# Optimization experiments

Measured on AMD Instinct MI355X. Metric: run time of the kernel, lower is better.

## Reference

```python
import jax, jax.numpy as jnp
import numpy as np

N_NODES = 100000
N_EDGES = 3200000
IN_CH = 32
HID = 16


def setup_inputs() -> dict:
    key = jax.random.key(0)
    ks = jax.random.split(key, 8)
    x = jax.random.normal(ks[0], (N_NODES, IN_CH), dtype=jnp.float32)
    edge_index = jax.random.randint(ks[1], (2, N_EDGES), 0, N_NODES, dtype=jnp.int64)
    s1 = 1.0 / np.sqrt(IN_CH)
    s2 = 1.0 / np.sqrt(HID)
    Wl1 = jax.random.normal(ks[2], (HID, IN_CH), dtype=jnp.float32) * s1
    Wr1 = jax.random.normal(ks[3], (HID, IN_CH), dtype=jnp.float32) * s1
    b1 = jnp.zeros((HID,), dtype=jnp.float32)
    Wl2 = jax.random.normal(ks[4], (1, HID), dtype=jnp.float32) * s2
    Wr2 = jax.random.normal(ks[5], (1, HID), dtype=jnp.float32) * s2
    b2 = jnp.zeros((1,), dtype=jnp.float32)
    return {"x": x, "edge_index": edge_index, "Wl1": Wl1, "Wr1": Wr1,
            "b1": b1, "Wl2": Wl2, "Wr2": Wr2, "b2": b2}


def _sage_conv(h, src, dst, deg_inv, Wl, Wr, b):
    # mean aggregation of source features at destination nodes
    msg_sum = jax.ops.segment_sum(h[src], dst, num_segments=N_NODES)  # [N, F]
    agg = msg_sum * deg_inv[:, None]
    # lin_l(agg) + lin_r(h): lin_l carries the bias (PyG SAGEConv convention)
    return agg @ Wl.T + b + h @ Wr.T


def reference(x, edge_index, Wl1, Wr1, b1, Wl2, Wr2, b2):
    src = edge_index[0]
    dst = edge_index[1]
    deg = jax.ops.segment_sum(jnp.ones((N_EDGES,), dtype=x.dtype), dst,
                              num_segments=N_NODES)
    deg_inv = 1.0 / jnp.maximum(deg, 1.0)  # mean; nodes w/o in-edges get 0 agg

    h = _sage_conv(x, src, dst, deg_inv, Wl1, Wr1, b1)
    h = jax.nn.relu(h)
    # F.dropout in eval mode -> identity
    out = _sage_conv(h, src, dst, deg_inv, Wl2, Wr2, b2)
    return out.squeeze(-1)  # [N]
```

## Files before the change

### kernel.cpp

```cpp
#include <hip/hip_runtime.h>

#define N_NODES 100000
#define N_EDGES 3200000
#define NB 1024
#define BKN 98
#define RSZ 3968
#define TILE 6250
#define NTILES 512
#define MAXIT 13
#define MAXB 8


__device__ __forceinline__ float bf2f_lo(unsigned int w) {
  return __uint_as_float(w << 16);
}
__device__ __forceinline__ float bf2f_hi(unsigned int w) {
  return __uint_as_float(w & 0xFFFF0000u);
}
__device__ __forceinline__ unsigned short f2bf(float f) {
  unsigned int b = __float_as_uint(f);
  return (unsigned short)((b + 0x7FFFu + ((b >> 16) & 1u)) >> 16);
}

__global__ __launch_bounds__(256) void k_proj1(
    const float* __restrict__ x, const float* __restrict__ Wl1,
    const float* __restrict__ Wr1, const float* __restrict__ b1,
    unsigned short* __restrict__ p1h, float* __restrict__ q1b,
    int* __restrict__ gcur) {
  __shared__ float sWl[512];
  __shared__ float sWr[512];
  __shared__ float sb[16];
  const int t = threadIdx.x;
  if (t < 64) {
    const int gi = blockIdx.x * 64 + t;
    if (gi < NB * 16) gcur[gi] = 0;
  }
  for (int i = t; i < 512; i += 256) {
    sWl[i] = Wl1[i];
    sWr[i] = Wr1[i];
  }
  if (t < 16) sb[t] = b1[t];
  __syncthreads();

  const int n = blockIdx.x * 256 + t;
  if (n >= N_NODES) return;

  float xr[32];
  const float4* xp = (const float4*)(x + (size_t)n * 32);
#pragma unroll
  for (int j = 0; j < 8; ++j) {
    float4 v = xp[j];
    xr[4 * j + 0] = v.x;
    xr[4 * j + 1] = v.y;
    xr[4 * j + 2] = v.z;
    xr[4 * j + 3] = v.w;
  }
  float pv[16], qv[16];
#pragma unroll
  for (int hh = 0; hh < 16; ++hh) {
    float a = 0.f, b = 0.f;
#pragma unroll
    for (int i = 0; i < 32; ++i) {
      a = fmaf(xr[i], sWl[hh * 32 + i], a);
      b = fmaf(xr[i], sWr[hh * 32 + i], b);
    }
    pv[hh] = a;
    qv[hh] = b + sb[hh];
  }
  unsigned int w[8];
#pragma unroll
  for (int j = 0; j < 8; ++j)
    w[j] = (unsigned int)f2bf(pv[2 * j]) |
           ((unsigned int)f2bf(pv[2 * j + 1]) << 16);
  uint4* pp = (uint4*)(p1h + (size_t)n * 16);
  pp[0] = make_uint4(w[0], w[1], w[2], w[3]);
  pp[1] = make_uint4(w[4], w[5], w[6], w[7]);
  float4* qp = (float4*)(q1b + (size_t)n * 16);
#pragma unroll
  for (int j = 0; j < 4; ++j)
    qp[j] = make_float4(qv[4 * j], qv[4 * j + 1], qv[4 * j + 2], qv[4 * j + 3]);
}

__global__ __launch_bounds__(512) void k_bscatter(const int* __restrict__ ei,
                                                  int* __restrict__ gcur,
                                                  int* __restrict__ recs) {
  __shared__ int hist[1024];
  __shared__ int delta[NB];
  __shared__ int seg[512];
  __shared__ int stage[TILE];
  __shared__ unsigned short bid[TILE + 6];
  const int t = threadIdx.x;
  for (int i = t; i < 1024; i += 512) hist[i] = 0;
  __syncthreads();

  const int tb = blockIdx.x * TILE;
  int rec[MAXIT], aux[MAXIT];
#pragma unroll
  for (int i = 0; i < MAXIT; ++i) {
    const int pos = t + i * 512;
    if (pos < TILE) {
      const int e = tb + pos;
      const int s = ei[e];
      const int d = ei[N_EDGES + e];
      const int k = (int)((unsigned)d / (unsigned)BKN);
      const int rank = atomicAdd(&hist[k], 1);
      rec[i] = ((d - k * BKN) << 17) | s;
      aux[i] = (k << 16) | rank;
    } else {
      aux[i] = -1;
    }
  }
  __syncthreads();

  const int s0 = hist[2 * t], s1 = hist[2 * t + 1];
  const int my = s0 + s1;
  seg[t] = my;
  __syncthreads();
#pragma unroll
  for (int o = 1; o < 512; o <<= 1) {
    const int a = (t >= o) ? seg[t - o] : 0;
    __syncthreads();
    seg[t] += a;
    __syncthreads();
  }
  const int ex = seg[t] - my;
  hist[2 * t] = ex;
  hist[2 * t + 1] = ex + s0;
  {
    const int b = 2 * t;
    if (s0) delta[b] = b * RSZ + atomicAdd(&gcur[b * 16], s0) - ex;
    if (s1)
      delta[b + 1] =
          (b + 1) * RSZ + atomicAdd(&gcur[(b + 1) * 16], s1) - (ex + s0);
  }
  __syncthreads();

#pragma unroll
  for (int i = 0; i < MAXIT; ++i) {
    if (aux[i] >= 0) stage[hist[aux[i] >> 16] + (aux[i] & 0xFFFF)] = rec[i];
  }
  for (int k2 = t; k2 < NB; k2 += 512) {
    const int st = hist[k2];
    const int en = (k2 == NB - 1) ? TILE : hist[k2 + 1];
    for (int p = st; p < en; ++p) bid[p] = (unsigned short)k2;
  }
  __syncthreads();

  for (int pos = t; pos < TILE; pos += 512) {
    const int bb = bid[pos];
    const int idx = delta[bb] + pos;
    if (idx < (bb + 1) * RSZ) recs[idx] = stage[pos];
  }
}

__global__ __launch_bounds__(512, 8) void k_sortagg1(
    const int* __restrict__ gcur, const int* __restrict__ recs,
    const unsigned short* __restrict__ p1h, const float* __restrict__ q1b,
    const float* __restrict__ Wl2, const float* __restrict__ Wr2,
    float* __restrict__ p2, float* __restrict__ r2,
    float* __restrict__ deg_inv) {
  __shared__ int hist[128];
  __shared__ int nstart[128];
  __shared__ int ssort[RSZ];
  __shared__ float sWl[16], sWr[16];
  const int t = threadIdx.x;
  const int kb = blockIdx.x;
  const int b0 = kb * RSZ;
  const int gend = b0 + min(gcur[kb * 16], RSZ);
  if (t < 128) hist[t] = 0;
  if (t < 16) {
    sWl[t] = Wl2[t];
    sWr[t] = Wr2[t];
  }
  __syncthreads();

  int rc[MAXB], ax[MAXB];
#pragma unroll
  for (int i = 0; i < MAXB; ++i) {
    const int r = b0 + t + i * 512;
    if (r < gend) {
      const int rv = recs[r];
      const int local = rv >> 17;
      const int rank = atomicAdd(&hist[local], 1);
      rc[i] = rv & 0x1FFFF;
      ax[i] = (local << 13) | rank;
    } else {
      ax[i] = -1;
    }
  }
  __syncthreads();

  {
    const int v = (t < 128) ? hist[t] : 0;
    if (t < 128) nstart[t] = v;
    __syncthreads();
#pragma unroll
    for (int o = 1; o < 128; o <<= 1) {
      const int a = (t < 128 && t >= o) ? nstart[t - o] : 0;
      __syncthreads();
      if (t < 128) nstart[t] += a;
      __syncthreads();
    }
    if (t < 128) nstart[t] -= v;
  }
  __syncthreads();

#pragma unroll
  for (int i = 0; i < MAXB; ++i) {
    if (ax[i] >= 0) ssort[nstart[ax[i] >> 13] + (ax[i] & 0x1FFF)] = rc[i];
  }
  __syncthreads();

  const int quad = t & 3;
  const int half = quad & 1;
  const int epar = quad >> 1;
  const unsigned short* pb = p1h + half * 8;
  const int local = t >> 2;
  if (local < BKN) {
    const int n = kb * BKN + local;
    if (n < N_NODES) {
      const int st = nstart[local];
      const int k = hist[local];

      float acc[8];
#pragma unroll
      for (int i = 0; i < 8; ++i) acc[i] = 0.f;
      int j = epar;
      for (; j + 6 < k; j += 8) {
        const int s0 = ssort[st + j], s1 = ssort[st + j + 2],
                  s2 = ssort[st + j + 4], s3 = ssort[st + j + 6];
        const uint4 w0 = *(const uint4*)(pb + (size_t)s0 * 16);
        const uint4 w1 = *(const uint4*)(pb + (size_t)s1 * 16);
        const uint4 w2 = *(const uint4*)(pb + (size_t)s2 * 16);
        const uint4 w3 = *(const uint4*)(pb + (size_t)s3 * 16);
        acc[0] +=
            (bf2f_lo(w0.x) + bf2f_lo(w1.x)) + (bf2f_lo(w2.x) + bf2f_lo(w3.x));
        acc[1] +=
            (bf2f_hi(w0.x) + bf2f_hi(w1.x)) + (bf2f_hi(w2.x) + bf2f_hi(w3.x));
        acc[2] +=
            (bf2f_lo(w0.y) + bf2f_lo(w1.y)) + (bf2f_lo(w2.y) + bf2f_lo(w3.y));
        acc[3] +=
            (bf2f_hi(w0.y) + bf2f_hi(w1.y)) + (bf2f_hi(w2.y) + bf2f_hi(w3.y));
        acc[4] +=
            (bf2f_lo(w0.z) + bf2f_lo(w1.z)) + (bf2f_lo(w2.z) + bf2f_lo(w3.z));
        acc[5] +=
            (bf2f_hi(w0.z) + bf2f_hi(w1.z)) + (bf2f_hi(w2.z) + bf2f_hi(w3.z));
        acc[6] +=
            (bf2f_lo(w0.w) + bf2f_lo(w1.w)) + (bf2f_lo(w2.w) + bf2f_lo(w3.w));
        acc[7] +=
            (bf2f_hi(w0.w) + bf2f_hi(w1.w)) + (bf2f_hi(w2.w) + bf2f_hi(w3.w));
      }
      for (; j < k; j += 2) {
        const uint4 w = *(const uint4*)(pb + (size_t)ssort[st + j] * 16);
        acc[0] += bf2f_lo(w.x);
        acc[1] += bf2f_hi(w.x);
        acc[2] += bf2f_lo(w.y);
        acc[3] += bf2f_hi(w.y);
        acc[4] += bf2f_lo(w.z);
        acc[5] += bf2f_hi(w.z);
        acc[6] += bf2f_lo(w.w);
        acc[7] += bf2f_hi(w.w);
      }
#pragma unroll
      for (int i = 0; i < 8; ++i) acc[i] += __shfl_xor(acc[i], 2);

      const float di = 1.f / fmaxf((float)k, 1.f);
      const float4* qp = (const float4*)(q1b + (size_t)n * 16 + half * 8);
      const float4 qa = qp[0], qb = qp[1];
      float h[8];
      h[0] = fmaxf(fmaf(acc[0], di, qa.x), 0.f);
      h[1] = fmaxf(fmaf(acc[1], di, qa.y), 0.f);
      h[2] = fmaxf(fmaf(acc[2], di, qa.z), 0.f);
      h[3] = fmaxf(fmaf(acc[3], di, qa.w), 0.f);
      h[4] = fmaxf(fmaf(acc[4], di, qb.x), 0.f);
      h[5] = fmaxf(fmaf(acc[5], di, qb.y), 0.f);
      h[6] = fmaxf(fmaf(acc[6], di, qb.z), 0.f);
      h[7] = fmaxf(fmaf(acc[7], di, qb.w), 0.f);
      float pa = 0.f, pbv = 0.f;
#pragma unroll
      for (int i = 0; i < 8; ++i) {
        pa = fmaf(h[i], sWl[half * 8 + i], pa);
        pbv = fmaf(h[i], sWr[half * 8 + i], pbv);
      }
      pa += __shfl_xor(pa, 1);
      pbv += __shfl_xor(pbv, 1);
      if (quad == 0) {
        p2[n] = pa;
        r2[n] = pbv;
        deg_inv[n] = di;
      }
    }
  }
}

__global__ __launch_bounds__(512, 8) void k_agg2out(
    const int* __restrict__ gcur, const int* __restrict__ recs,
    const float* __restrict__ p2, const float* __restrict__ r2,
    const float* __restrict__ deg_inv, const float* __restrict__ b2,
    float* __restrict__ out) {
  __shared__ float acc[BKN];
  const int t = threadIdx.x;
  const int kb = blockIdx.x;
  if (t < BKN) acc[t] = 0.f;
  __syncthreads();

  const int b0 = kb * RSZ;
  const int cnt = min(gcur[kb * 16], RSZ);
  int r = t;
  for (; r + 1536 < cnt; r += 2048) {
    const int rv0 = recs[b0 + r];
    const int rv1 = recs[b0 + r + 512];
    const int rv2 = recs[b0 + r + 1024];
    const int rv3 = recs[b0 + r + 1536];
    const float v0 = p2[rv0 & 0x1FFFF];
    const float v1 = p2[rv1 & 0x1FFFF];
    const float v2 = p2[rv2 & 0x1FFFF];
    const float v3 = p2[rv3 & 0x1FFFF];
    atomicAdd(&acc[rv0 >> 17], v0);
    atomicAdd(&acc[rv1 >> 17], v1);
    atomicAdd(&acc[rv2 >> 17], v2);
    atomicAdd(&acc[rv3 >> 17], v3);
  }
  for (; r < cnt; r += 512) {
    const int rv = recs[b0 + r];
    atomicAdd(&acc[rv >> 17], p2[rv & 0x1FFFF]);
  }
  __syncthreads();

  if (t < BKN) {
    const int n = kb * BKN + t;
    if (n < N_NODES) out[n] = fmaf(acc[t], deg_inv[n], r2[n] + b2[0]);
  }
}

extern "C" void kernel_launch(void* const* d_in, const int* in_sizes, int n_in,
                              void* d_out, int out_size, void* d_ws,
                              size_t ws_size, hipStream_t stream) {
  const float* x   = (const float*)d_in[0];
  const int*   ei  = (const int*)d_in[1];
  const float* Wl1 = (const float*)d_in[2];
  const float* Wr1 = (const float*)d_in[3];
  const float* b1  = (const float*)d_in[4];
  const float* Wl2 = (const float*)d_in[5];
  const float* Wr2 = (const float*)d_in[6];
  const float* b2  = (const float*)d_in[7];
  float* out = (float*)d_out;

  const size_t N = N_NODES;
  int* wi = (int*)d_ws;
  int* gcur = wi;
  int* recs = wi + NB * 16;
  unsigned short* p1h = (unsigned short*)(recs + (size_t)NB * RSZ);
  float* q1b     = (float*)(p1h + 16 * N);
  float* p2      = q1b + 16 * N;
  float* r2      = p2 + N;
  float* deg_inv = r2 + N;

  k_proj1<<<(N_NODES + 255) / 256, 256, 0, stream>>>(x, Wl1, Wr1, b1, p1h,
                                                     q1b, gcur);
  k_bscatter<<<NTILES, 512, 0, stream>>>(ei, gcur, recs);
  k_sortagg1<<<NB, 512, 0, stream>>>(gcur, recs, p1h, q1b, Wl2, Wr2, p2, r2,
                                     deg_inv);
  k_agg2out<<<NB, 512, 0, stream>>>(gcur, recs, p2, r2, deg_inv, b2, out);
}
```

Before: 172.0 us.

## Fuse projection with edge scatter and merge layer aggregations via grid barrier

Layer-1 projection and the bucket scatter now run as one launch: one group of blocks scatters edges while another group projects nodes. The two aggregation stages are merged into a cooperative kernel that uses a global atomic barrier, so the sorted source lists, r2 and deg_inv stay in shared memory and are not written out and read back. The gcur reset moves to a memset, and the 128-entry prefix scan now uses wave shuffles. This removes two launches and some global traffic, but adds a spin-wait grid barrier and the memset, and falls back to the old path if the cooperative launch fails.

Measured after the change: 356.7 us. 107% more time.

```diff
diff --git a/kernel.cpp b/kernel.cpp
--- a/kernel.cpp
+++ b/kernel.cpp
@@ -9,6 +9,7 @@
 #define NTILES 512
 #define MAXIT 13
 #define MAXB 8
+#define PROJ_BLOCKS 196
 
 
 __device__ __forceinline__ float bf2f_lo(unsigned int w) {
@@ -17,32 +18,101 @@
 __device__ __forceinline__ float bf2f_hi(unsigned int w) {
   return __uint_as_float(w & 0xFFFF0000u);
 }
-__device__ __forceinline__ unsigned short f2bf(float f) {
+__device__ __forceinline__ unsigned int f2bf(float f) {
   unsigned int b = __float_as_uint(f);
-  return (unsigned short)((b + 0x7FFFu + ((b >> 16) & 1u)) >> 16);
-}
-
-__global__ __launch_bounds__(256) void k_proj1(
-    const float* __restrict__ x, const float* __restrict__ Wl1,
-    const float* __restrict__ Wr1, const float* __restrict__ b1,
-    unsigned short* __restrict__ p1h, float* __restrict__ q1b,
-    int* __restrict__ gcur) {
-  __shared__ float sWl[512];
-  __shared__ float sWr[512];
-  __shared__ float sb[16];
+  return (b + 0x7FFFu + ((b >> 16) & 1u)) >> 16;
+}
+
+__global__ __launch_bounds__(512, 8) void k_scatterproj(
+    const float* __restrict__ x, const int* __restrict__ ei,
+    const float* __restrict__ Wl1, const float* __restrict__ Wr1,
+    const float* __restrict__ b1, unsigned short* __restrict__ p1h,
+    float* __restrict__ q1b, int* __restrict__ gcur, int* __restrict__ recs) {
+  __shared__ union {
+    struct {
+      int hist[1024];
+      int delta[NB];
+      int seg[512];
+      int stage[TILE];
+      unsigned short bid[TILE + 6];
+    } s;
+    struct { float Wl[512], Wr[512], b[16]; } w;
+  } u;
   const int t = threadIdx.x;
-  if (t < 64) {
-    const int gi = blockIdx.x * 64 + t;
-    if (gi < NB * 16) gcur[gi] = 0;
-  }
-  for (int i = t; i < 512; i += 256) {
-    sWl[i] = Wl1[i];
-    sWr[i] = Wr1[i];
-  }
-  if (t < 16) sb[t] = b1[t];
-  __syncthreads();
-
-  const int n = blockIdx.x * 256 + t;
+  const int kb = blockIdx.x;
+
+  if (kb < NTILES) {
+    for (int i = t; i < 1024; i += 512) u.s.hist[i] = 0;
+    __syncthreads();
+
+    const int tb = kb * TILE;
+    int rec[MAXIT], aux[MAXIT];
+#pragma unroll
+    for (int i = 0; i < MAXIT; ++i) {
+      const int pos = t + i * 512;
+      if (pos < TILE) {
+        const int e = tb + pos;
+        const int s = ei[e];
+        const int d = ei[N_EDGES + e];
+        const int k = (int)((unsigned)d / (unsigned)BKN);
+        const int rank = atomicAdd(&u.s.hist[k], 1);
+        rec[i] = ((d - k * BKN) << 17) | s;
+        aux[i] = (k << 16) | rank;
+      } else {
+        aux[i] = -1;
+      }
+    }
+    __syncthreads();
+
+    const int s0 = u.s.hist[2 * t], s1 = u.s.hist[2 * t + 1];
+    const int my = s0 + s1;
+    u.s.seg[t] = my;
+    __syncthreads();
+#pragma unroll
+    for (int o = 1; o < 512; o <<= 1) {
+      const int a = (t >= o) ? u.s.seg[t - o] : 0;
+      __syncthreads();
+      u.s.seg[t] += a;
+      __syncthreads();
+    }
+    const int ex = u.s.seg[t] - my;
+    u.s.hist[2 * t] = ex;
+    u.s.hist[2 * t + 1] = ex + s0;
+    {
+      const int b = 2 * t;
+      if (s0) u.s.delta[b] = b * RSZ + atomicAdd(&gcur[b * 16], s0) - ex;
+      if (s1)
+        u.s.delta[b + 1] =
+            (b + 1) * RSZ + atomicAdd(&gcur[(b + 1) * 16], s1) - (ex + s0);
+    }
+    __syncthreads();
+
+#pragma unroll
+    for (int i = 0; i < MAXIT; ++i) {
+      if (aux[i] >= 0)
+        u.s.stage[u.s.hist[aux[i] >> 16] + (aux[i] & 0xFFFF)] = rec[i];
+    }
+    for (int k2 = t; k2 < NB; k2 += 512) {
+      const int st = u.s.hist[k2];
+      const int en = (k2 == NB - 1) ? TILE : u.s.hist[k2 + 1];
+      for (int p = st; p < en; ++p) u.s.bid[p] = (unsigned short)k2;
+    }
+    __syncthreads();
+
+    for (int pos = t; pos < TILE; pos += 512) {
+      const int bb = u.s.bid[pos];
+      const int idx = u.s.delta[bb] + pos;
+      if (idx < (bb + 1) * RSZ) recs[idx] = u.s.stage[pos];
+    }
+    return;
+  }
+
+  u.w.Wl[t] = Wl1[t];
+  u.w.Wr[t] = Wr1[t];
+  if (t < 16) u.w.b[t] = b1[t];
+  __syncthreads();
+
+  const int n = (kb - NTILES) * 512 + t;
   if (n >= N_NODES) return;
 
   float xr[32];
@@ -55,116 +125,40 @@
     xr[4 * j + 2] = v.z;
     xr[4 * j + 3] = v.w;
   }
-  float pv[16], qv[16];
-#pragma unroll
-  for (int hh = 0; hh < 16; ++hh) {
-    float a = 0.f, b = 0.f;
-#pragma unroll
-    for (int i = 0; i < 32; ++i) {
-      a = fmaf(xr[i], sWl[hh * 32 + i], a);
-      b = fmaf(xr[i], sWr[hh * 32 + i], b);
-    }
-    pv[hh] = a;
-    qv[hh] = b + sb[hh];
-  }
-  unsigned int w[8];
-#pragma unroll
-  for (int j = 0; j < 8; ++j)
-    w[j] = (unsigned int)f2bf(pv[2 * j]) |
-           ((unsigned int)f2bf(pv[2 * j + 1]) << 16);
-  uint4* pp = (uint4*)(p1h + (size_t)n * 16);
-  pp[0] = make_uint4(w[0], w[1], w[2], w[3]);
-  pp[1] = make_uint4(w[4], w[5], w[6], w[7]);
-  float4* qp = (float4*)(q1b + (size_t)n * 16);
-#pragma unroll
-  for (int j = 0; j < 4; ++j)
-    qp[j] = make_float4(qv[4 * j], qv[4 * j + 1], qv[4 * j + 2], qv[4 * j + 3]);
-}
-
-__global__ __launch_bounds__(512) void k_bscatter(const int* __restrict__ ei,
-                                                  int* __restrict__ gcur,
-                                                  int* __restrict__ recs) {
-  __shared__ int hist[1024];
-  __shared__ int delta[NB];
-  __shared__ int seg[512];
-  __shared__ int stage[TILE];
-  __shared__ unsigned short bid[TILE + 6];
-  const int t = threadIdx.x;
-  for (int i = t; i < 1024; i += 512) hist[i] = 0;
-  __syncthreads();
-
-  const int tb = blockIdx.x * TILE;
-  int rec[MAXIT], aux[MAXIT];
-#pragma unroll
-  for (int i = 0; i < MAXIT; ++i) {
-    const int pos = t + i * 512;
-    if (pos < TILE) {
-      const int e = tb + pos;
-      const int s = ei[e];
-      const int d = ei[N_EDGES + e];
-      const int k = (int)((unsigned)d / (unsigned)BKN);
-      const int rank = atomicAdd(&hist[k], 1);
-      rec[i] = ((d - k * BKN) << 17) | s;
-      aux[i] = (k << 16) | rank;
-    } else {
-      aux[i] = -1;
-    }
-  }
-  __syncthreads();
-
-  const int s0 = hist[2 * t], s1 = hist[2 * t + 1];
-  const int my = s0 + s1;
-  seg[t] = my;
-  __syncthreads();
-#pragma unroll
-  for (int o = 1; o < 512; o <<= 1) {
-    const int a = (t >= o) ? seg[t - o] : 0;
-    __syncthreads();
-    seg[t] += a;
-    __syncthreads();
-  }
-  const int ex = seg[t] - my;
-  hist[2 * t] = ex;
-  hist[2 * t + 1] = ex + s0;
-  {
-    const int b = 2 * t;
-    if (s0) delta[b] = b * RSZ + atomicAdd(&gcur[b * 16], s0) - ex;
-    if (s1)
-      delta[b + 1] =
-          (b + 1) * RSZ + atomicAdd(&gcur[(b + 1) * 16], s1) - (ex + s0);
-  }
-  __syncthreads();
-
-#pragma unroll
-  for (int i = 0; i < MAXIT; ++i) {
-    if (aux[i] >= 0) stage[hist[aux[i] >> 16] + (aux[i] & 0xFFFF)] = rec[i];
-  }
-  for (int k2 = t; k2 < NB; k2 += 512) {
-    const int st = hist[k2];
-    const int en = (k2 == NB - 1) ? TILE : hist[k2 + 1];
-    for (int p = st; p < en; ++p) bid[p] = (unsigned short)k2;
-  }
-  __syncthreads();
-
-  for (int pos = t; pos < TILE; pos += 512) {
-    const int bb = bid[pos];
-    const int idx = delta[bb] + pos;
-    if (idx < (bb + 1) * RSZ) recs[idx] = stage[pos];
-  }
-}
-
-__global__ __launch_bounds__(512, 8) void k_sortagg1(
-    const int* __restrict__ gcur, const int* __restrict__ recs,
-    const unsigned short* __restrict__ p1h, const float* __restrict__ q1b,
-    const float* __restrict__ Wl2, const float* __restrict__ Wr2,
-    float* __restrict__ p2, float* __restrict__ r2,
-    float* __restrict__ deg_inv) {
-  __shared__ int hist[128];
-  __shared__ int nstart[128];
-  __shared__ int ssort[RSZ];
-  __shared__ float sWl[16], sWr[16];
-  const int t = threadIdx.x;
-  const int kb = blockIdx.x;
+#pragma unroll
+  for (int ch = 0; ch < 2; ++ch) {
+    float pv[8], qv[8];
+#pragma unroll
+    for (int h2 = 0; h2 < 8; ++h2) {
+      const int hh = ch * 8 + h2;
+      float a = 0.f, b = 0.f;
+#pragma unroll
+      for (int i = 0; i < 32; ++i) {
+        a = fmaf(xr[i], u.w.Wl[hh * 32 + i], a);
+        b = fmaf(xr[i], u.w.Wr[hh * 32 + i], b);
+      }
+      pv[h2] = a;
+      qv[h2] = b + u.w.b[hh];
+    }
+    unsigned int w[4];
+#pragma unroll
+    for (int j = 0; j < 4; ++j)
+      w[j] = f2bf(pv[2 * j]) | (f2bf(pv[2 * j + 1]) << 16);
+    ((uint4*)(p1h + (size_t)n * 16))[ch] = make_uint4(w[0], w[1], w[2], w[3]);
+    float4* qp = (float4*)(q1b + (size_t)n * 16) + 2 * ch;
+    qp[0] = make_float4(qv[0], qv[1], qv[2], qv[3]);
+    qp[1] = make_float4(qv[4], qv[5], qv[6], qv[7]);
+  }
+}
+
+template <bool FUSED>
+__device__ __forceinline__ void sortagg_body(
+    const int t, const int kb, const int* __restrict__ gcur,
+    const int* __restrict__ recs, const unsigned short* __restrict__ p1h,
+    const float* __restrict__ q1b, const float* __restrict__ Wl2,
+    const float* __restrict__ Wr2, float* __restrict__ p2,
+    float* __restrict__ r2g, float* __restrict__ degg, int* hist, int* nstart,
+    int* ssort, float* sWl, float* sWr, float* sr2, float* sdi) {
   const int b0 = kb * RSZ;
   const int gend = b0 + min(gcur[kb * 16], RSZ);
   if (t < 128) hist[t] = 0;
@@ -190,18 +184,21 @@
   }
   __syncthreads();
 
-  {
-    const int v = (t < 128) ? hist[t] : 0;
-    if (t < 128) nstart[t] = v;
-    __syncthreads();
-#pragma unroll
-    for (int o = 1; o < 128; o <<= 1) {
-      const int a = (t < 128 && t >= o) ? nstart[t - o] : 0;
-      __syncthreads();
-      if (t < 128) nstart[t] += a;
-      __syncthreads();
-    }
-    if (t < 128) nstart[t] -= v;
+  if (t < 64) {
+    const int a = hist[t], b = hist[t + 64];
+    int ia = a, ib = b;
+#pragma unroll
+    for (int o = 1; o < 64; o <<= 1) {
+      const int ua = __shfl_up(ia, o);
+      const int ub = __shfl_up(ib, o);
+      if (t >= o) {
+        ia += ua;
+        ib += ub;
+      }
+    }
+    const int tt = __shfl(ia, 63);
+    nstart[t] = ia - a;
+    nstart[t + 64] = tt + ib - b;
   }
   __syncthreads();
 
@@ -286,11 +283,78 @@
       pbv += __shfl_xor(pbv, 1);
       if (quad == 0) {
         p2[n] = pa;
-        r2[n] = pbv;
-        deg_inv[n] = di;
-      }
-    }
-  }
+        if (FUSED) {
+          sr2[local] = pbv;
+          sdi[local] = di;
+        } else {
+          r2g[n] = pbv;
+          degg[n] = di;
+        }
+      }
+    }
+  }
+}
+
+__global__ __launch_bounds__(512, 8) void k_mid(
+    const int* __restrict__ gcur, const int* __restrict__ recs,
+    const unsigned short* __restrict__ p1h, const float* __restrict__ q1b,
+    const float* __restrict__ Wl2, const float* __restrict__ Wr2,
+    float* __restrict__ p2, const float* __restrict__ b2,
+    float* __restrict__ out, int* __restrict__ bar) {
+  __shared__ int hist[128], nstart[128];
+  __shared__ int ssort[RSZ];
+  __shared__ float sWl[16], sWr[16], sr2[BKN], sdi[BKN];
+  const int t = threadIdx.x;
+  const int kb = blockIdx.x;
+
+  sortagg_body<true>(t, kb, gcur, recs, p1h, q1b, Wl2, Wr2, p2, nullptr,
+                     nullptr, hist, nstart, ssort, sWl, sWr, sr2, sdi);
+
+  __syncthreads();
+  if (t == 0) {
+    __threadfence();
+    __hip_atomic_fetch_add(bar, 1, __ATOMIC_RELEASE, __HIP_MEMORY_SCOPE_AGENT);
+    while (__hip_atomic_load(bar, __ATOMIC_RELAXED, __HIP_MEMORY_SCOPE_AGENT) <
+           NB) {
+      __builtin_amdgcn_s_sleep(8);
+    }
+    __threadfence();
+  }
+  __syncthreads();
+
+  const int lane4 = t & 3;
+  const int local = t >> 2;
+  if (local < BKN) {
+    const int n = kb * BKN + local;
+    if (n < N_NODES) {
+      const int st = nstart[local];
+      const int k = hist[local];
+      float u = 0.f;
+      int j = lane4;
+      for (; j + 4 < k; j += 8) {
+        const int a = ssort[st + j], b = ssort[st + j + 4];
+        u += p2[a] + p2[b];
+      }
+      for (; j < k; j += 4) u += p2[ssort[st + j]];
+      u += __shfl_xor(u, 1);
+      u += __shfl_xor(u, 2);
+      if (lane4 == 0) out[n] = fmaf(u, sdi[local], sr2[local] + b2[0]);
+    }
+  }
+}
+
+__global__ __launch_bounds__(512, 8) void k_sortagg1(
+    const int* __restrict__ gcur, const int* __restrict__ recs,
+    const unsigned short* __restrict__ p1h, const float* __restrict__ q1b,
+    const float* __restrict__ Wl2, const float* __restrict__ Wr2,
+    float* __restrict__ p2, float* __restrict__ r2,
+    float* __restrict__ deg_inv) {
+  __shared__ int hist[128], nstart[128];
+  __shared__ int ssort[RSZ];
+  __shared__ float sWl[16], sWr[16];
+  sortagg_body<false>(threadIdx.x, blockIdx.x, gcur, recs, p1h, q1b, Wl2, Wr2,
+                      p2, r2, deg_inv, hist, nstart, ssort, sWl, sWr, nullptr,
+                      nullptr);
 }
 
 __global__ __launch_bounds__(512, 8) void k_agg2out(
@@ -349,17 +413,28 @@
   const size_t N = N_NODES;
   int* wi = (int*)d_ws;
   int* gcur = wi;
-  int* recs = wi + NB * 16;
+  int* bar  = wi + NB * 16;
+  int* recs = bar + 16;
   unsigned short* p1h = (unsigned short*)(recs + (size_t)NB * RSZ);
   float* q1b     = (float*)(p1h + 16 * N);
   float* p2      = q1b + 16 * N;
   float* r2      = p2 + N;
   float* deg_inv = r2 + N;
 
-  k_proj1<<<(N_NODES + 255) / 256, 256, 0, stream>>>(x, Wl1, Wr1, b1, p1h,
-                                                     q1b, gcur);
-  k_bscatter<<<NTILES, 512, 0, stream>>>(ei, gcur, recs);
-  k_sortagg1<<<NB, 512, 0, stream>>>(gcur, recs, p1h, q1b, Wl2, Wr2, p2, r2,
-                                     deg_inv);
-  k_agg2out<<<NB, 512, 0, stream>>>(gcur, recs, p2, r2, deg_inv, b2, out);
-}
+  hipMemsetAsync(gcur, 0, (NB * 16 + 16) * sizeof(int), stream);
+  k_scatterproj<<<NTILES + PROJ_BLOCKS, 512, 0, stream>>>(x, ei, Wl1, Wr1, b1,
+                                                          p1h, q1b, gcur,
+                                                          recs);
+
+  void* ka[] = {(void*)&gcur, (void*)&recs, (void*)&p1h, (void*)&q1b,
+                (void*)&Wl2,  (void*)&Wr2,  (void*)&p2,  (void*)&b2,
+                (void*)&out,  (void*)&bar};
+  hipError_t err = hipLaunchCooperativeKernel(
+      reinterpret_cast<void*>(k_mid), dim3(NB), dim3(512), ka, 0, stream);
+  if (err != hipSuccess) {
+    (void)hipGetLastError();
+    k_sortagg1<<<NB, 512, 0, stream>>>(gcur, recs, p1h, q1b, Wl2, Wr2, p2, r2,
+                                       deg_inv);
+    k_agg2out<<<NB, 512, 0, stream>>>(gcur, recs, p2, r2, deg_inv, b2, out);
+  }
+}
```
